# Kernel tuning notes

Measured on AMD Instinct MI355X. Metric: run time of the kernel, lower is better.

Reference implementation:

```python
import jax, jax.numpy as jnp
import numpy as np

KH, KW = 15, 15
H, W = 4096, 4096


def setup_inputs() -> dict:
    key = jax.random.key(0)
    kx, kw = jax.random.split(key)
    x = jax.random.normal(kx, (H, W), dtype=jnp.float32)
    weight = jax.random.uniform(kw, (KH, KW), dtype=jnp.float32)
    bias = jnp.zeros((1,), dtype=jnp.float32)
    return {"x": x, "weight": weight, "bias": bias}


def reference(x, weight, bias):
    # corr2d: valid 2D cross-correlation of [H,W] input with [kh,kw] kernel,
    # output [H-kh+1, W-kw+1], plus scalar bias.
    lhs = x[None, None, :, :]            # [1,1,H,W]
    rhs = weight[None, None, :, :]       # [1,1,kh,kw]
    out = jax.lax.conv_general_dilated(
        lhs, rhs,
        window_strides=(1, 1),
        padding="VALID",
        dimension_numbers=("NCHW", "OIHW", "NCHW"),
    )[0, 0]                              # [H-kh+1, W-kw+1]
    return out + bias[0]
```

## Files before the change

### kernel.cpp

```cpp
#include <hip/hip_runtime.h>

typedef short bf16x8 __attribute__((ext_vector_type(8)));
typedef float f32x4  __attribute__((ext_vector_type(4)));

static constexpr int KH = 15, KW = 15;
static constexpr int HI = 4096, WI = 4096;
static constexpr int HO = HI - KH + 1, WO = WI - KW + 1;
static constexpr int TM = 64, TN = 128;
static constexpr int LR   = TM + KH - 1;
static constexpr int LC   = TN + 16;
static constexpr int LSTR = 152;

__device__ __forceinline__ unsigned int f2bf(float f) {
  unsigned int u = __builtin_bit_cast(unsigned int, f);
  return (u + 0x7FFFu + ((u >> 16) & 1u)) >> 16;
}

__global__ __launch_bounds__(512, 8)
void conv2d_mfma2(const float* __restrict__ x, const float* __restrict__ w,
                  const float* __restrict__ bias, float* __restrict__ out) {
  __shared__ unsigned short sx[LR * LSTR];
  __shared__ unsigned short btab[15 * 64 * 8];

  const int tid  = threadIdx.x;
  const int row0 = blockIdx.y * TM;
  const int col0 = blockIdx.x * TN;

  for (int i = tid; i < 15 * 64; i += 512) {
    const int kh = i >> 6;
    const int l  = i & 63;
    const int j  = l & 15;
    const int p0 = (l >> 4) * 8;
    unsigned int d[4];
    #pragma unroll
    for (int t2 = 0; t2 < 4; ++t2) {
      const int idx0 = p0 + 2 * t2 - j;
      const int idx1 = idx0 + 1;
      const unsigned int b0 = (idx0 >= 0 && idx0 < KW) ? f2bf(w[kh * KW + idx0]) : 0u;
      const unsigned int b1 = (idx1 >= 0 && idx1 < KW) ? f2bf(w[kh * KW + idx1]) : 0u;
      d[t2] = b0 | (b1 << 16);
    }
    *(uint4*)&btab[i * 8] = make_uint4(d[0], d[1], d[2], d[3]);
  }

  for (int i = tid; i < LR * (LC / 4); i += 512) {
    const int r  = i / (LC / 4);
    const int c4 = (i - r * (LC / 4)) * 4;
    const int gr = row0 + r;
    const int gc = col0 + c4;
    float4 v = make_float4(0.f, 0.f, 0.f, 0.f);
    if (gr < HI) {
      const float* p = &x[(long)gr * WI + gc];
      if (gc + 3 < WI) {
        v = *(const float4*)p;
      } else {
        if (gc + 0 < WI) v.x = p[0];
        if (gc + 1 < WI) v.y = p[1];
        if (gc + 2 < WI) v.z = p[2];
        if (gc + 3 < WI) v.w = p[3];
      }
    }
    unsigned int lo = f2bf(v.x) | (f2bf(v.y) << 16);
    unsigned int hi = f2bf(v.z) | (f2bf(v.w) << 16);
    *(uint2*)&sx[r * LSTR + c4] = make_uint2(lo, hi);
  }

  const float bs = bias[0];
  __syncthreads();

  const int lane = tid & 63;
  const int wv   = tid >> 6;
  const int arow = lane & 15;
  const int acol = wv * 16 + (lane >> 4) * 8;
  const unsigned short* abase = &sx[arow * LSTR + acol];
  const unsigned short* bbase = &btab[lane * 8];

  f32x4 acc[4];
  #pragma unroll
  for (int m = 0; m < 4; ++m) acc[m] = (f32x4){0.f, 0.f, 0.f, 0.f};

  #pragma unroll
  for (int kh = 0; kh < 15; ++kh) {
    const bf16x8 b = *(const bf16x8*)(bbase + kh * 64 * 8);
    #pragma unroll
    for (int m = 0; m < 4; ++m) {
      bf16x8 a = *(const bf16x8*)(abase + (16 * m + kh) * LSTR);
      acc[m] = __builtin_amdgcn_mfma_f32_16x16x32_bf16(a, b, acc[m], 0, 0, 0);
    }
  }

  const int ocol = col0 + wv * 16 + (lane & 15);
  if (ocol < WO) {
    #pragma unroll
    for (int m = 0; m < 4; ++m) {
      const int orow0 = row0 + 16 * m + (lane >> 4) * 4;
      #pragma unroll
      for (int r = 0; r < 4; ++r) {
        const int orow = orow0 + r;
        if (orow < HO) out[(long)orow * WO + ocol] = acc[m][r] + bs;
      }
    }
  }
}

extern "C" void kernel_launch(void* const* d_in, const int* in_sizes, int n_in,
                              void* d_out, int out_size, void* d_ws, size_t ws_size,
                              hipStream_t stream) {
  const float* x    = (const float*)d_in[0];
  const float* w    = (const float*)d_in[1];
  const float* bias = (const float*)d_in[2];
  float* out        = (float*)d_out;

  dim3 grid((WO + TN - 1) / TN, (HO + TM - 1) / TM);
  conv2d_mfma2<<<grid, dim3(512, 1, 1), 0, stream>>>(x, w, bias, out);
}
```

Measured before the change: 38.91 us.

## Make blocks persistent over four row tiles with double-buffered LDS prefetch

Each block now processes four vertically stacked 64-row tiles instead of one. The next tile's global loads are issued into registers before the current tile's MFMA work, then written into a second LDS buffer. The weight fragments are built once per block and kept in registers for all tiles. Conversion to bf16 uses the packed v_cvt_pk_bf16_f32 instruction. This is meant to hide global load latency and amortize the weight-table setup, at the cost of more registers and LDS, lower occupancy (launch bounds 4), and a grid with a quarter as many blocks.

Result: slower. 42.61 us (+9.5%).

```diff
diff --git a/kernel.cpp b/kernel.cpp
--- a/kernel.cpp
+++ b/kernel.cpp
@@ -7,24 +7,70 @@
 static constexpr int HI = 4096, WI = 4096;
 static constexpr int HO = HI - KH + 1, WO = WI - KW + 1;
 static constexpr int TM = 64, TN = 128;
+static constexpr int NT = 4;
 static constexpr int LR   = TM + KH - 1;
 static constexpr int LC   = TN + 16;
 static constexpr int LSTR = 152;
+static constexpr int IPR   = LC / 4;
+static constexpr int ITEMS = LR * IPR;
+static constexpr int SITER = (ITEMS + 511) / 512;
 
 __device__ __forceinline__ unsigned int f2bf(float f) {
   unsigned int u = __builtin_bit_cast(unsigned int, f);
   return (u + 0x7FFFu + ((u >> 16) & 1u)) >> 16;
 }
 
-__global__ __launch_bounds__(512, 8)
-void conv2d_mfma2(const float* __restrict__ x, const float* __restrict__ w,
+__device__ __forceinline__ unsigned int cvt_pk_bf16(float lo, float hi) {
+  unsigned int r;
+  asm("v_cvt_pk_bf16_f32 %0, %1, %2" : "=v"(r) : "v"(lo), "v"(hi));
+  return r;
+}
+
+__device__ __forceinline__ float4 load_item(const float* __restrict__ x,
+                                            int row0, int col0, int it) {
+  float4 v = make_float4(0.f, 0.f, 0.f, 0.f);
+  if (it < ITEMS) {
+    const int r  = it / IPR;
+    const int c4 = (it - r * IPR) * 4;
+    const int gr = row0 + r;
+    const int gc = col0 + c4;
+    if (gr < HI) {
+      const float* p = &x[(long)gr * WI + gc];
+      if (gc + 3 < WI) {
+        v = *(const float4*)p;
+      } else {
+        if (gc + 0 < WI) v.x = p[0];
+        if (gc + 1 < WI) v.y = p[1];
+        if (gc + 2 < WI) v.z = p[2];
+        if (gc + 3 < WI) v.w = p[3];
+      }
+    }
+  }
+  return v;
+}
+
+__device__ __forceinline__ void write_item(unsigned short* sx, int it, float4 v) {
+  if (it < ITEMS) {
+    const int r  = it / IPR;
+    const int c4 = (it - r * IPR) * 4;
+    uint2 d = make_uint2(cvt_pk_bf16(v.x, v.y), cvt_pk_bf16(v.z, v.w));
+    *(uint2*)&sx[r * LSTR + c4] = d;
+  }
+}
+
+__global__ __launch_bounds__(512, 4)
+void conv2d_mfma3(const float* __restrict__ x, const float* __restrict__ w,
                   const float* __restrict__ bias, float* __restrict__ out) {
-  __shared__ unsigned short sx[LR * LSTR];
+  __shared__ unsigned short sx[2][LR * LSTR];
   __shared__ unsigned short btab[15 * 64 * 8];
 
-  const int tid  = threadIdx.x;
-  const int row0 = blockIdx.y * TM;
-  const int col0 = blockIdx.x * TN;
+  const int tid   = threadIdx.x;
+  const int col0  = blockIdx.x * TN;
+  const int srow0 = blockIdx.y * (NT * TM);
+
+  float4 v[SITER];
+  #pragma unroll
+  for (int k = 0; k < SITER; ++k) v[k] = load_item(x, srow0, col0, tid + 512 * k);
 
   for (int i = tid; i < 15 * 64; i += 512) {
     const int kh = i >> 6;
@@ -43,27 +89,8 @@
     *(uint4*)&btab[i * 8] = make_uint4(d[0], d[1], d[2], d[3]);
   }
 
-  for (int i = tid; i < LR * (LC / 4); i += 512) {
-    const int r  = i / (LC / 4);
-    const int c4 = (i - r * (LC / 4)) * 4;
-    const int gr = row0 + r;
-    const int gc = col0 + c4;
-    float4 v = make_float4(0.f, 0.f, 0.f, 0.f);
-    if (gr < HI) {
-      const float* p = &x[(long)gr * WI + gc];
-      if (gc + 3 < WI) {
-        v = *(const float4*)p;
-      } else {
-        if (gc + 0 < WI) v.x = p[0];
-        if (gc + 1 < WI) v.y = p[1];
-        if (gc + 2 < WI) v.z = p[2];
-        if (gc + 3 < WI) v.w = p[3];
-      }
-    }
-    unsigned int lo = f2bf(v.x) | (f2bf(v.y) << 16);
-    unsigned int hi = f2bf(v.z) | (f2bf(v.w) << 16);
-    *(uint2*)&sx[r * LSTR + c4] = make_uint2(lo, hi);
-  }
+  #pragma unroll
+  for (int k = 0; k < SITER; ++k) write_item(&sx[0][0], tid + 512 * k, v[k]);
 
   const float bs = bias[0];
   __syncthreads();
@@ -72,34 +99,56 @@
   const int wv   = tid >> 6;
   const int arow = lane & 15;
   const int acol = wv * 16 + (lane >> 4) * 8;
-  const unsigned short* abase = &sx[arow * LSTR + acol];
-  const unsigned short* bbase = &btab[lane * 8];
 
-  f32x4 acc[4];
+  bf16x8 bfrag[15];
   #pragma unroll
-  for (int m = 0; m < 4; ++m) acc[m] = (f32x4){0.f, 0.f, 0.f, 0.f};
+  for (int kh = 0; kh < 15; ++kh)
+    bfrag[kh] = *(const bf16x8*)&btab[(kh * 64 + lane) * 8];
 
-  #pragma unroll
-  for (int kh = 0; kh < 15; ++kh) {
-    const bf16x8 b = *(const bf16x8*)(bbase + kh * 64 * 8);
+  int cur = 0;
+  for (int t = 0; t < NT; ++t) {
+    const int row0 = srow0 + t * TM;
+
+    if (t + 1 < NT) {
+      #pragma unroll
+      for (int k = 0; k < SITER; ++k)
+        v[k] = load_item(x, row0 + TM, col0, tid + 512 * k);
+    }
+
+    const unsigned short* abase = &sx[cur][arow * LSTR + acol];
+    f32x4 acc[4];
     #pragma unroll
-    for (int m = 0; m < 4; ++m) {
-      bf16x8 a = *(const bf16x8*)(abase + (16 * m + kh) * LSTR);
-      acc[m] = __builtin_amdgcn_mfma_f32_16x16x32_bf16(a, b, acc[m], 0, 0, 0);
-    }
-  }
+    for (int m = 0; m < 4; ++m) acc[m] = (f32x4){0.f, 0.f, 0.f, 0.f};
 
-  const int ocol = col0 + wv * 16 + (lane & 15);
-  if (ocol < WO) {
     #pragma unroll
-    for (int m = 0; m < 4; ++m) {
-      const int orow0 = row0 + 16 * m + (lane >> 4) * 4;
+    for (int kh = 0; kh < 15; ++kh) {
       #pragma unroll
-      for (int r = 0; r < 4; ++r) {
-        const int orow = orow0 + r;
-        if (orow < HO) out[(long)orow * WO + ocol] = acc[m][r] + bs;
+      for (int m = 0; m < 4; ++m) {
+        bf16x8 a = *(const bf16x8*)(abase + (16 * m + kh) * LSTR);
+        acc[m] = __builtin_amdgcn_mfma_f32_16x16x32_bf16(a, bfrag[kh], acc[m], 0, 0, 0);
       }
     }
+
+    const int ocol = col0 + wv * 16 + (lane & 15);
+    if (ocol < WO) {
+      #pragma unroll
+      for (int m = 0; m < 4; ++m) {
+        const int orow0 = row0 + 16 * m + (lane >> 4) * 4;
+        #pragma unroll
+        for (int r = 0; r < 4; ++r) {
+          const int orow = orow0 + r;
+          if (orow < HO) out[(long)orow * WO + ocol] = acc[m][r] + bs;
+        }
+      }
+    }
+
+    if (t + 1 < NT) {
+      #pragma unroll
+      for (int k = 0; k < SITER; ++k)
+        write_item(&sx[cur ^ 1][0], tid + 512 * k, v[k]);
+    }
+    __syncthreads();
+    cur ^= 1;
   }
 }
 
@@ -111,6 +160,6 @@
   const float* bias = (const float*)d_in[2];
   float* out        = (float*)d_out;
 
-  dim3 grid((WO + TN - 1) / TN, (HO + TM - 1) / TM);
-  conv2d_mfma2<<<grid, dim3(512, 1, 1), 0, stream>>>(x, w, bias, out);
+  dim3 grid((WO + TN - 1) / TN, HI / (NT * TM));
+  conv2d_mfma3<<<grid, dim3(512, 1, 1), 0, stream>>>(x, w, bias, out);
 }
```

## Reuse A-fragments via DPP row rotation instead of per-kh LDS reloads

Applied to the files above, without the earlier changes.

The kernel now loads five 16-row A fragments from LDS once per wave. For each kernel row it builds the shifted fragments with DPP row-rotate and a per-lane select, replacing 60 LDS vector loads per wave with register shuffles. The f32-to-bf16 packing uses the v_cvt_pk_bf16_f32 instruction, and the launch bound drops to 4 blocks/SM. The LDS tile is padded to 80 rows so the fifth fragment load stays in bounds, though those padding rows are never written. This adds DPP/select VALU work and register pressure, which can lower occupancy.

New measurement: 45.45 us. 1.17x slower.

```diff
diff --git a/kernel.cpp b/kernel.cpp
--- a/kernel.cpp
+++ b/kernel.cpp
@@ -8,18 +8,47 @@
 static constexpr int HO = HI - KH + 1, WO = WI - KW + 1;
 static constexpr int TM = 64, TN = 128;
 static constexpr int LR   = TM + KH - 1;
+static constexpr int LRA  = 80;
 static constexpr int LC   = TN + 16;
 static constexpr int LSTR = 152;
+static constexpr int IPR  = LC / 4;
 
 __device__ __forceinline__ unsigned int f2bf(float f) {
   unsigned int u = __builtin_bit_cast(unsigned int, f);
   return (u + 0x7FFFu + ((u >> 16) & 1u)) >> 16;
 }
 
-__global__ __launch_bounds__(512, 8)
-void conv2d_mfma2(const float* __restrict__ x, const float* __restrict__ w,
-                  const float* __restrict__ bias, float* __restrict__ out) {
-  __shared__ unsigned short sx[LR * LSTR];
+__device__ __forceinline__ unsigned int cvt_pk_bf16(float lo, float hi) {
+  unsigned int r;
+  asm("v_cvt_pk_bf16_f32 %0, %1, %2" : "=v"(r) : "v"(lo), "v"(hi));
+  return r;
+}
+
+template<int CTRL>
+__device__ __forceinline__ int4 dpp_ror(int4 s) {
+  int4 r;
+  r.x = __builtin_amdgcn_update_dpp(s.x, s.x, CTRL, 0xF, 0xF, false);
+  r.y = __builtin_amdgcn_update_dpp(s.y, s.y, CTRL, 0xF, 0xF, false);
+  r.z = __builtin_amdgcn_update_dpp(s.z, s.z, CTRL, 0xF, 0xF, false);
+  r.w = __builtin_amdgcn_update_dpp(s.w, s.w, CTRL, 0xF, 0xF, false);
+  return r;
+}
+
+__device__ __forceinline__ int4 sel4(bool c, int4 a, int4 b) {
+  int4 r;
+  r.x = c ? a.x : b.x;  r.y = c ? a.y : b.y;
+  r.z = c ? a.z : b.z;  r.w = c ? a.w : b.w;
+  return r;
+}
+
+__device__ __forceinline__ bf16x8 bc(int4 v) { return __builtin_bit_cast(bf16x8, v); }
+
+#define MFMA(a, b, c) __builtin_amdgcn_mfma_f32_16x16x32_bf16((a), (b), (c), 0, 0, 0)
+
+__global__ __launch_bounds__(512, 4)
+void conv2d_dpp(const float* __restrict__ x, const float* __restrict__ w,
+                const float* __restrict__ bias, float* __restrict__ out) {
+  __shared__ unsigned short sx[LRA * LSTR];
   __shared__ unsigned short btab[15 * 64 * 8];
 
   const int tid  = threadIdx.x;
@@ -43,9 +72,9 @@
     *(uint4*)&btab[i * 8] = make_uint4(d[0], d[1], d[2], d[3]);
   }
 
-  for (int i = tid; i < LR * (LC / 4); i += 512) {
-    const int r  = i / (LC / 4);
-    const int c4 = (i - r * (LC / 4)) * 4;
+  for (int i = tid; i < LR * IPR; i += 512) {
+    const int r  = i / IPR;
+    const int c4 = (i - r * IPR) * 4;
     const int gr = row0 + r;
     const int gc = col0 + c4;
     float4 v = make_float4(0.f, 0.f, 0.f, 0.f);
@@ -60,9 +89,7 @@
         if (gc + 3 < WI) v.w = p[3];
       }
     }
-    unsigned int lo = f2bf(v.x) | (f2bf(v.y) << 16);
-    unsigned int hi = f2bf(v.z) | (f2bf(v.w) << 16);
-    *(uint2*)&sx[r * LSTR + c4] = make_uint2(lo, hi);
+    *(uint2*)&sx[r * LSTR + c4] = make_uint2(cvt_pk_bf16(v.x, v.y), cvt_pk_bf16(v.z, v.w));
   }
 
   const float bs = bias[0];
@@ -70,34 +97,58 @@
 
   const int lane = tid & 63;
   const int wv   = tid >> 6;
-  const int arow = lane & 15;
+  const int q    = lane & 15;
   const int acol = wv * 16 + (lane >> 4) * 8;
-  const unsigned short* abase = &sx[arow * LSTR + acol];
+  const unsigned short* sbase = &sx[q * LSTR + acol];
   const unsigned short* bbase = &btab[lane * 8];
 
-  f32x4 acc[4];
-  #pragma unroll
-  for (int m = 0; m < 4; ++m) acc[m] = (f32x4){0.f, 0.f, 0.f, 0.f};
+  int4 s0 = *(const int4*)(sbase + 0  * 16 * LSTR);
+  int4 s1 = *(const int4*)(sbase + 1  * 16 * LSTR);
+  int4 s2 = *(const int4*)(sbase + 2  * 16 * LSTR);
+  int4 s3 = *(const int4*)(sbase + 3  * 16 * LSTR);
+  int4 s4 = *(const int4*)(sbase + 4  * 16 * LSTR);
 
-  #pragma unroll
-  for (int kh = 0; kh < 15; ++kh) {
-    const bf16x8 b = *(const bf16x8*)(bbase + kh * 64 * 8);
+  f32x4 acc0 = {0.f,0.f,0.f,0.f}, acc1 = {0.f,0.f,0.f,0.f};
+  f32x4 acc2 = {0.f,0.f,0.f,0.f}, acc3 = {0.f,0.f,0.f,0.f};
+
+  {
+    bf16x8 b = *(const bf16x8*)bbase;
+    acc0 = MFMA(bc(s0), b, acc0);
+    acc1 = MFMA(bc(s1), b, acc1);
+    acc2 = MFMA(bc(s2), b, acc2);
+    acc3 = MFMA(bc(s3), b, acc3);
+  }
+
+  #define KH_STEP(K)                                                          \
+  {                                                                           \
+    int4 r0 = dpp_ror<0x120 + 16 - (K)>(s0);                                  \
+    int4 r1 = dpp_ror<0x120 + 16 - (K)>(s1);                                  \
+    int4 r2 = dpp_ror<0x120 + 16 - (K)>(s2);                                  \
+    int4 r3 = dpp_ror<0x120 + 16 - (K)>(s3);                                  \
+    int4 r4 = dpp_ror<0x120 + 16 - (K)>(s4);                                  \
+    const bool w_ = (q + (K)) >= 16;                                          \
+    bf16x8 b = *(const bf16x8*)(bbase + (K) * 512);                           \
+    acc0 = MFMA(bc(sel4(w_, r1, r0)), b, acc0);                               \
+    acc1 = MFMA(bc(sel4(w_, r2, r1)), b, acc1);                               \
+    acc2 = MFMA(bc(sel4(w_, r3, r2)), b, acc2);                               \
+    acc3 = MFMA(bc(sel4(w_, r4, r3)), b, acc3);                               \
+  }
+
+  KH_STEP(1)  KH_STEP(2)  KH_STEP(3)  KH_STEP(4)  KH_STEP(5)
+  KH_STEP(6)  KH_STEP(7)  KH_STEP(8)  KH_STEP(9)  KH_STEP(10)
+  KH_STEP(11) KH_STEP(12) KH_STEP(13) KH_STEP(14)
+  #undef KH_STEP
+
+  const int ocol = col0 + wv * 16 + q;
+  if (ocol < WO) {
+    const int orb = row0 + (lane >> 4) * 4;
+    f32x4 av[4] = {acc0, acc1, acc2, acc3};
     #pragma unroll
     for (int m = 0; m < 4; ++m) {
-      bf16x8 a = *(const bf16x8*)(abase + (16 * m + kh) * LSTR);
-      acc[m] = __builtin_amdgcn_mfma_f32_16x16x32_bf16(a, b, acc[m], 0, 0, 0);
-    }
-  }
-
-  const int ocol = col0 + wv * 16 + (lane & 15);
-  if (ocol < WO) {
-    #pragma unroll
-    for (int m = 0; m < 4; ++m) {
-      const int orow0 = row0 + 16 * m + (lane >> 4) * 4;
       #pragma unroll
       for (int r = 0; r < 4; ++r) {
-        const int orow = orow0 + r;
-        if (orow < HO) out[(long)orow * WO + ocol] = acc[m][r] + bs;
+        const int orow = orb + 16 * m + r;
+        if (orow < HO) out[(long)orow * WO + ocol] = av[m][r] + bs;
       }
     }
   }
@@ -112,5 +163,5 @@
   float* out        = (float*)d_out;
 
   dim3 grid((WO + TN - 1) / TN, (HO + TM - 1) / TM);
-  conv2d_mfma2<<<grid, dim3(512, 1, 1), 0, stream>>>(x, w, bias, out);
+  conv2d_dpp<<<grid, dim3(512, 1, 1), 0, stream>>>(x, w, bias, out);
 }
```

## Switch to 32x32x16 MFMA with a Toeplitz weight table, larger tiles, XCD block remapping

Applied to the files above, without the earlier changes.

Replaces the 16x16x32 MFMA Toeplitz formulation with 32x32x16 bf16 MFMAs. Each wave computes two 32x32 output tiles that share the diagonal weight slots, and the output tile grows to 128x128. Block IDs are remapped so neighbouring tiles land on the same XCD, bf16 packing uses the hardware v_cvt_pk_bf16_f32 instruction, and the bias is folded into the accumulator init. The aim is to raise MFMA work per LDS load and cut the halo overhead per output. The cost is fewer resident blocks per CU and more complex index mapping.

After: 45.07 us. 15.8% more time.

```diff
diff --git a/kernel.cpp b/kernel.cpp
--- a/kernel.cpp
+++ b/kernel.cpp
@@ -1,51 +1,66 @@
 #include <hip/hip_runtime.h>
 
 typedef short bf16x8 __attribute__((ext_vector_type(8)));
-typedef float f32x4  __attribute__((ext_vector_type(4)));
+typedef float f32x16 __attribute__((ext_vector_type(16)));
 
 static constexpr int KH = 15, KW = 15;
 static constexpr int HI = 4096, WI = 4096;
 static constexpr int HO = HI - KH + 1, WO = WI - KW + 1;
-static constexpr int TM = 64, TN = 128;
+static constexpr int TM = 128, TN = 128;
 static constexpr int LR   = TM + KH - 1;
-static constexpr int LC   = TN + 16;
+static constexpr int LCS  = 148;
 static constexpr int LSTR = 152;
+static constexpr int IPR  = LCS / 4;
+static constexpr int ITEMS = LR * IPR;
+static constexpr int NSLOT = 72;
 
 __device__ __forceinline__ unsigned int f2bf(float f) {
   unsigned int u = __builtin_bit_cast(unsigned int, f);
   return (u + 0x7FFFu + ((u >> 16) & 1u)) >> 16;
 }
 
-__global__ __launch_bounds__(512, 8)
-void conv2d_mfma2(const float* __restrict__ x, const float* __restrict__ w,
-                  const float* __restrict__ bias, float* __restrict__ out) {
+__device__ __forceinline__ unsigned int cvt_pk_bf16(float lo, float hi) {
+  unsigned int r;
+  asm("v_cvt_pk_bf16_f32 %0, %1, %2" : "=v"(r) : "v"(lo), "v"(hi));
+  return r;
+}
+
+#define MFMA32(a, b, c) __builtin_amdgcn_mfma_f32_32x32x16_bf16((a), (b), (c), 0, 0, 0)
+
+__global__ __launch_bounds__(512, 4)
+void conv2d_mfma32(const float* __restrict__ x, const float* __restrict__ w,
+                   const float* __restrict__ bias, float* __restrict__ out) {
   __shared__ unsigned short sx[LR * LSTR];
-  __shared__ unsigned short btab[15 * 64 * 8];
+  __shared__ unsigned short btab[KH * NSLOT * 8];
 
-  const int tid  = threadIdx.x;
-  const int row0 = blockIdx.y * TM;
-  const int col0 = blockIdx.x * TN;
+  const int tid = threadIdx.x;
 
-  for (int i = tid; i < 15 * 64; i += 512) {
-    const int kh = i >> 6;
-    const int l  = i & 63;
-    const int j  = l & 15;
-    const int p0 = (l >> 4) * 8;
-    unsigned int d[4];
+  const int nwg  = gridDim.x * gridDim.y;
+  const int cpx  = nwg >> 3;
+  const int bid0 = blockIdx.y * gridDim.x + blockIdx.x;
+  const int bid  = (bid0 % 8) * cpx + (bid0 / 8);
+  const int row0 = (bid / 32) * TM;
+  const int col0 = (bid % 32) * TN;
+
+  for (int i = tid; i < KH * NSLOT; i += 512) {
+    const int kh = i / NSLOT;
+    const int d  = i - kh * NSLOT;
+    const int e0 = d - 31;
+    unsigned int dw[4];
     #pragma unroll
     for (int t2 = 0; t2 < 4; ++t2) {
-      const int idx0 = p0 + 2 * t2 - j;
-      const int idx1 = idx0 + 1;
-      const unsigned int b0 = (idx0 >= 0 && idx0 < KW) ? f2bf(w[kh * KW + idx0]) : 0u;
-      const unsigned int b1 = (idx1 >= 0 && idx1 < KW) ? f2bf(w[kh * KW + idx1]) : 0u;
-      d[t2] = b0 | (b1 << 16);
+      const int c0 = e0 + 2 * t2;
+      const int c1 = c0 + 1;
+      const unsigned int b0 = (c0 >= 0 && c0 < KW) ? f2bf(w[kh * KW + c0]) : 0u;
+      const unsigned int b1 = (c1 >= 0 && c1 < KW) ? f2bf(w[kh * KW + c1]) : 0u;
+      dw[t2] = b0 | (b1 << 16);
     }
-    *(uint4*)&btab[i * 8] = make_uint4(d[0], d[1], d[2], d[3]);
+    *(uint4*)&btab[i * 8] = make_uint4(dw[0], dw[1], dw[2], dw[3]);
   }
 
-  for (int i = tid; i < LR * (LC / 4); i += 512) {
-    const int r  = i / (LC / 4);
-    const int c4 = (i - r * (LC / 4)) * 4;
+  for (int i = tid; i < ITEMS; i += 512) {
+    const int r  = i / IPR;
+    const int c4 = (i - r * IPR) * 4;
     const int gr = row0 + r;
     const int gc = col0 + c4;
     float4 v = make_float4(0.f, 0.f, 0.f, 0.f);
@@ -60,9 +75,7 @@
         if (gc + 3 < WI) v.w = p[3];
       }
     }
-    unsigned int lo = f2bf(v.x) | (f2bf(v.y) << 16);
-    unsigned int hi = f2bf(v.z) | (f2bf(v.w) << 16);
-    *(uint2*)&sx[r * LSTR + c4] = make_uint2(lo, hi);
+    *(uint2*)&sx[r * LSTR + c4] = make_uint2(cvt_pk_bf16(v.x, v.y), cvt_pk_bf16(v.z, v.w));
   }
 
   const float bs = bias[0];
@@ -70,35 +83,46 @@
 
   const int lane = tid & 63;
   const int wv   = tid >> 6;
-  const int arow = lane & 15;
-  const int acol = wv * 16 + (lane >> 4) * 8;
-  const unsigned short* abase = &sx[arow * LSTR + acol];
-  const unsigned short* bbase = &btab[lane * 8];
+  const int g    = wv >> 1;
+  const int p    = wv & 1;
+  const int n    = lane & 31;
+  const int kg   = lane >> 5;
 
-  f32x4 acc[4];
+  const unsigned short* abase = &sx[(32 * g + n) * LSTR + 64 * p + 8 * kg];
+  const unsigned short* bbase = &btab[(8 * kg - n + 31) * 8];
+
+  f32x16 acc0, acc1;
   #pragma unroll
-  for (int m = 0; m < 4; ++m) acc[m] = (f32x4){0.f, 0.f, 0.f, 0.f};
+  for (int r = 0; r < 16; ++r) { acc0[r] = bs; acc1[r] = 0.f; }
 
   #pragma unroll
-  for (int kh = 0; kh < 15; ++kh) {
-    const bf16x8 b = *(const bf16x8*)(bbase + kh * 64 * 8);
-    #pragma unroll
-    for (int m = 0; m < 4; ++m) {
-      bf16x8 a = *(const bf16x8*)(abase + (16 * m + kh) * LSTR);
-      acc[m] = __builtin_amdgcn_mfma_f32_16x16x32_bf16(a, b, acc[m], 0, 0, 0);
-    }
+  for (int kh = 0; kh < KH; ++kh) {
+    const unsigned short* ar = abase + kh * LSTR;
+    const bf16x8 a0 = *(const bf16x8*)(ar + 0);
+    const bf16x8 a1 = *(const bf16x8*)(ar + 16);
+    const bf16x8 a2 = *(const bf16x8*)(ar + 32);
+    const bf16x8 a3 = *(const bf16x8*)(ar + 48);
+    const bf16x8 a4 = *(const bf16x8*)(ar + 64);
+    const unsigned short* br = bbase + kh * (NSLOT * 8);
+    const bf16x8 b0 = *(const bf16x8*)(br + 0);
+    const bf16x8 b1 = *(const bf16x8*)(br + 128);
+    const bf16x8 b2 = *(const bf16x8*)(br + 256);
+    acc0 = MFMA32(a0, b0, acc0);
+    acc0 = MFMA32(a1, b1, acc0);
+    acc0 = MFMA32(a2, b2, acc0);
+    acc1 = MFMA32(a2, b0, acc1);
+    acc1 = MFMA32(a3, b1, acc1);
+    acc1 = MFMA32(a4, b2, acc1);
   }
 
-  const int ocol = col0 + wv * 16 + (lane & 15);
-  if (ocol < WO) {
-    #pragma unroll
-    for (int m = 0; m < 4; ++m) {
-      const int orow0 = row0 + 16 * m + (lane >> 4) * 4;
-      #pragma unroll
-      for (int r = 0; r < 4; ++r) {
-        const int orow = orow0 + r;
-        if (orow < HO) out[(long)orow * WO + ocol] = acc[m][r] + bs;
-      }
+  const int oc  = col0 + 64 * p + n;
+  const int orb = row0 + 32 * g + 4 * kg;
+  #pragma unroll
+  for (int r = 0; r < 16; ++r) {
+    const int orow = orb + (r & 3) + 8 * (r >> 2);
+    if (orow < HO) {
+      if (oc < WO)      out[(long)orow * WO + oc]      = acc0[r];
+      if (oc + 32 < WO) out[(long)orow * WO + oc + 32] = acc1[r] + bs;
     }
   }
 }
@@ -112,5 +136,5 @@
   float* out        = (float*)d_out;
 
   dim3 grid((WO + TN - 1) / TN, (HO + TM - 1) / TM);
-  conv2d_mfma2<<<grid, dim3(512, 1, 1), 0, stream>>>(x, w, bias, out);
+  conv2d_mfma32<<<grid, dim3(512, 1, 1), 0, stream>>>(x, w, bias, out);
 }
```
